# Kernel tuning notes

Measured on AMD Instinct MI355X. Metric: run time of the kernel, lower is better.

Reference implementation:

```python
import jax, jax.numpy as jnp
import numpy as np

W = 4           # cp_size (simulated ranks)
NUM_HEADS = 32
HEAD_SIZE = 128
NUM_KV_HEADS = 8
BLOCK_SIZE = 16
NUM_BLOCKS = 1024
MAX_BLOCKS = 32
MAX_CTX = 512   # <= _PARTITION_SIZE so single-partition stats are exact
NUM_SEQS = 32
SCALE = 1.0 / np.sqrt(HEAD_SIZE)
NEG_INF = -1e30


def setup_inputs() -> dict:
    key = jax.random.key(0)
    k1, k2, k3, k4, k5 = jax.random.split(key, 5)
    query = jax.random.normal(k1, (NUM_SEQS, 1, NUM_HEADS * HEAD_SIZE), dtype=jnp.float32)
    # per-rank paged KV caches, layout [W, num_blocks, kv_heads, block_size, head_size]
    key_cache = jax.random.normal(k2, (W, NUM_BLOCKS, NUM_KV_HEADS, BLOCK_SIZE, HEAD_SIZE), dtype=jnp.float32)
    value_cache = jax.random.normal(k3, (W, NUM_BLOCKS, NUM_KV_HEADS, BLOCK_SIZE, HEAD_SIZE), dtype=jnp.float32)
    block_tables = jax.random.randint(k4, (W, NUM_SEQS, MAX_BLOCKS), 0, NUM_BLOCKS, dtype=jnp.int32)
    context_lens = jax.random.randint(k5, (W, NUM_SEQS), 1, MAX_CTX + 1, dtype=jnp.int32)
    return {"query": query, "key_cache": key_cache, "value_cache": value_cache,
            "block_tables": block_tables, "context_lens": context_lens}


def reference(query, key_cache, value_cache, block_tables, context_lens):
    B, L, _ = query.shape
    S = B * L                       # num_seqs (decode: L=1)
    G = NUM_KV_HEADS
    Q = NUM_HEADS // G              # queries per kv head
    T = MAX_BLOCKS * BLOCK_SIZE     # max context per rank

    q = query.reshape(S, G, Q, HEAD_SIZE)
    ridx = jnp.arange(W)[:, None, None]
    # gather paged blocks: [W, S, MAX_BLOCKS, G, BLOCK_SIZE, D] -> [W, S, G, T, D]
    k = key_cache[ridx, block_tables].transpose(0, 1, 3, 2, 4, 5).reshape(W, S, G, T, HEAD_SIZE)
    v = value_cache[ridx, block_tables].transpose(0, 1, 3, 2, 4, 5).reshape(W, S, G, T, HEAD_SIZE)

    logits = jnp.einsum('sgqd,wsgtd->wsgqt', q, k) * SCALE
    mask = jnp.arange(T)[None, None, None, None, :] < context_lens[:, :, None, None, None]
    logits = jnp.where(mask, logits, NEG_INF)

    # per-rank online-softmax stats (== paged_attention_v2 single-partition output)
    m = jnp.max(logits, axis=-1)                      # [W,S,G,Q] max logit per rank
    p = jnp.exp(logits - m[..., None])
    p = jnp.where(mask, p, 0.0)
    esum = jnp.sum(p, axis=-1)                        # [W,S,G,Q]
    out_r = jnp.einsum('wsgqt,wsgtd->wsgqd', p, v) / esum[..., None]  # normalized per-rank out

    # cross-rank log-sum-exp reduction (distributed_paged_attention_v2_reduce)
    gmax = jnp.max(m, axis=0)                         # [S,G,Q]
    w_r = esum * jnp.exp(m - gmax[None])              # [W,S,G,Q]
    out = jnp.sum(out_r * w_r[..., None], axis=0) / jnp.sum(w_r, axis=0)[..., None]

    return out.reshape(B, L, NUM_HEADS * HEAD_SIZE)
```

## Files before the change

### kernel.cpp

```cpp
#include <hip/hip_runtime.h>
#include <math.h>

#define W 4
#define NUM_HEADS 32
#define HEAD_SIZE 128
#define G 8
#define QPG 4
#define BLOCK_SZ 16
#define NUM_BLOCKS 1024
#define MAX_BLOCKS 32
#define S 32
#define SCALE 0.08838834764831845f

template <bool FUSED>
__global__ __launch_bounds__(256)
void pa_partial_kernel(const float* __restrict__ query,
                       const float* __restrict__ key_cache,
                       const float* __restrict__ value_cache,
                       const int* __restrict__ block_tables,
                       const int* __restrict__ context_lens,
                       float* __restrict__ acc_ws,
                       float* __restrict__ m_ws,
                       float* __restrict__ e_ws,
                       float* __restrict__ out)
{
    const int bx = blockIdx.x;
    int s, g, w0, w1;
    if (FUSED) {
        s = bx / G; g = bx % G; w0 = 0; w1 = W;
    } else {
        g = bx % G;
        int t = bx / G;
        s = t % S;
        w0 = t / S; w1 = w0 + 1;
    }
    const int tid   = threadIdx.x;
    const int accid = tid >> 5;
    const int lane  = tid & 31;
    const int d0    = lane * 4;

    __shared__ int   bt_lds[MAX_BLOCKS];
    __shared__ float sm_m[8][QPG];
    __shared__ float sm_e[8][QPG];
    __shared__ float sm_acc[8][QPG][HEAD_SIZE];

    float4 qf[QPG];
#pragma unroll
    for (int qi = 0; qi < QPG; ++qi)
        qf[qi] = *reinterpret_cast<const float4*>(
            query + ((size_t)s * NUM_HEADS + g * QPG + qi) * HEAD_SIZE + d0);

    float  m_i[QPG], e_i[QPG];
    float4 acc[QPG];
#pragma unroll
    for (int qi = 0; qi < QPG; ++qi) {
        m_i[qi] = -INFINITY; e_i[qi] = 0.f;
        acc[qi] = make_float4(0.f, 0.f, 0.f, 0.f);
    }

    const size_t stride_blk = (size_t)G * BLOCK_SZ * HEAD_SIZE;

    for (int w = w0; w < w1; ++w) {
        __syncthreads();
        if (tid < MAX_BLOCKS)
            bt_lds[tid] = block_tables[((size_t)w * S + s) * MAX_BLOCKS + tid];
        __syncthreads();

        const int ctx = context_lens[w * S + s];
        const float* kbase = key_cache   + ((size_t)w * NUM_BLOCKS * G + g) * BLOCK_SZ * HEAD_SIZE;
        const float* vbase = value_cache + ((size_t)w * NUM_BLOCKS * G + g) * BLOCK_SZ * HEAD_SIZE;

        for (int t = accid; t < ctx; t += 8) {
            const int blk  = bt_lds[t >> 4];
            const int slot = t & (BLOCK_SZ - 1);
            const size_t off = (size_t)blk * stride_blk + (size_t)slot * HEAD_SIZE + d0;
            const float4 kx = *reinterpret_cast<const float4*>(kbase + off);
            const float4 vx = *reinterpret_cast<const float4*>(vbase + off);

            float4 dv;
            dv.x = qf[0].x * kx.x + qf[0].y * kx.y + qf[0].z * kx.z + qf[0].w * kx.w;
            dv.y = qf[1].x * kx.x + qf[1].y * kx.y + qf[1].z * kx.z + qf[1].w * kx.w;
            dv.z = qf[2].x * kx.x + qf[2].y * kx.y + qf[2].z * kx.z + qf[2].w * kx.w;
            dv.w = qf[3].x * kx.x + qf[3].y * kx.y + qf[3].z * kx.z + qf[3].w * kx.w;
#pragma unroll
            for (int o = 16; o > 0; o >>= 1) {
                dv.x += __shfl_xor(dv.x, o);
                dv.y += __shfl_xor(dv.y, o);
                dv.z += __shfl_xor(dv.z, o);
                dv.w += __shfl_xor(dv.w, o);
            }
            const float lg[QPG] = {dv.x * SCALE, dv.y * SCALE, dv.z * SCALE, dv.w * SCALE};
#pragma unroll
            for (int qi = 0; qi < QPG; ++qi) {
                const float mn    = fmaxf(m_i[qi], lg[qi]);
                const float alpha = __expf(m_i[qi] - mn);
                const float p     = __expf(lg[qi] - mn);
                m_i[qi] = mn;
                e_i[qi] = e_i[qi] * alpha + p;
                acc[qi].x = acc[qi].x * alpha + p * vx.x;
                acc[qi].y = acc[qi].y * alpha + p * vx.y;
                acc[qi].z = acc[qi].z * alpha + p * vx.z;
                acc[qi].w = acc[qi].w * alpha + p * vx.w;
            }
        }
    }

#pragma unroll
    for (int qi = 0; qi < QPG; ++qi) {
        if (lane == 0) { sm_m[accid][qi] = m_i[qi]; sm_e[accid][qi] = e_i[qi]; }
        sm_acc[accid][qi][d0 + 0] = acc[qi].x;
        sm_acc[accid][qi][d0 + 1] = acc[qi].y;
        sm_acc[accid][qi][d0 + 2] = acc[qi].z;
        sm_acc[accid][qi][d0 + 3] = acc[qi].w;
    }
    __syncthreads();

    for (int p = tid; p < QPG * HEAD_SIZE; p += 256) {
        const int qi = p >> 7;
        const int d  = p & (HEAD_SIZE - 1);
        float gm = -INFINITY;
#pragma unroll
        for (int h = 0; h < 8; ++h) gm = fmaxf(gm, sm_m[h][qi]);
        float num = 0.f, den = 0.f;
#pragma unroll
        for (int h = 0; h < 8; ++h) {
            const float sc = __expf(sm_m[h][qi] - gm);
            num += sm_acc[h][qi][d] * sc;
            den += sm_e[h][qi] * sc;
        }
        if (FUSED) {
            out[((size_t)s * NUM_HEADS + g * QPG + qi) * HEAD_SIZE + d] = num / den;
        } else {
            const size_t idx = (((size_t)w0 * S + s) * G + g) * QPG + qi;
            acc_ws[idx * HEAD_SIZE + d] = num;
            if (d == 0) { m_ws[idx] = gm; e_ws[idx] = den; }
        }
    }
}

__global__ __launch_bounds__(256)
void pa_reduce_kernel(const float* __restrict__ acc_ws,
                      const float* __restrict__ m_ws,
                      const float* __restrict__ e_ws,
                      float* __restrict__ out)
{
    const int bx = blockIdx.x;
    const int s = bx / G, g = bx % G;
    const int tid = threadIdx.x;
    for (int p = tid; p < QPG * HEAD_SIZE; p += 256) {
        const int qi = p >> 7;
        const int d  = p & (HEAD_SIZE - 1);
        float mw[W], ew[W];
        float gm = -INFINITY;
#pragma unroll
        for (int w = 0; w < W; ++w) {
            const size_t idx = (((size_t)w * S + s) * G + g) * QPG + qi;
            mw[w] = m_ws[idx];
            ew[w] = e_ws[idx];
            gm = fmaxf(gm, mw[w]);
        }
        float num = 0.f, den = 0.f;
#pragma unroll
        for (int w = 0; w < W; ++w) {
            const float sc = __expf(mw[w] - gm);
            const size_t idx = (((size_t)w * S + s) * G + g) * QPG + qi;
            num += acc_ws[idx * HEAD_SIZE + d] * sc;
            den += ew[w] * sc;
        }
        out[((size_t)s * NUM_HEADS + g * QPG + qi) * HEAD_SIZE + d] = num / den;
    }
}

extern "C" void kernel_launch(void* const* d_in, const int* in_sizes, int n_in,
                              void* d_out, int out_size, void* d_ws, size_t ws_size,
                              hipStream_t stream) {
    const float* query       = (const float*)d_in[0];
    const float* key_cache   = (const float*)d_in[1];
    const float* value_cache = (const float*)d_in[2];
    const int*   block_tables = (const int*)d_in[3];
    const int*   context_lens = (const int*)d_in[4];
    float* out = (float*)d_out;

    const size_t n_acc   = (size_t)W * S * G * QPG * HEAD_SIZE;
    const size_t n_stats = (size_t)W * S * G * QPG;
    const size_t need    = (n_acc + 2 * n_stats) * sizeof(float);

    if (ws_size >= need) {
        float* acc_ws = (float*)d_ws;
        float* m_ws   = acc_ws + n_acc;
        float* e_ws   = m_ws + n_stats;
        pa_partial_kernel<false><<<W * S * G, 256, 0, stream>>>(
            query, key_cache, value_cache, block_tables, context_lens,
            acc_ws, m_ws, e_ws, nullptr);
        pa_reduce_kernel<<<S * G, 256, 0, stream>>>(acc_ws, m_ws, e_ws, out);
    } else {
        pa_partial_kernel<true><<<S * G, 256, 0, stream>>>(
            query, key_cache, value_cache, block_tables, context_lens,
            nullptr, nullptr, nullptr, out);
    }
}
```

Baseline: 471.5 us.

## Split each rank's context across two workgroups and process two tokens per iteration

The partial kernel now launches SPLIT=2 workgroups per (rank, seq, kv-head), each taking an interleaved half of the tokens, and the reduce kernel combines 8 partitions instead of 4. Each warp handles two tokens per loop iteration with one combined online-softmax update, so more loads are in flight and fewer exp/rescale operations run per token. Launch bounds request 5 blocks per CU for occupancy. The cost is a larger workspace, more partial-output traffic and a wider reduction. The fused fallback becomes a separate kernel.

Result: no change. 463.7 us (-1.6%).

```diff
diff --git a/kernel.cpp b/kernel.cpp
--- a/kernel.cpp
+++ b/kernel.cpp
@@ -10,10 +10,15 @@
 #define NUM_BLOCKS 1024
 #define MAX_BLOCKS 32
 #define S 32
+#define SPLIT 2
+#define NPART (W * SPLIT)
 #define SCALE 0.08838834764831845f
-
-template <bool FUSED>
-__global__ __launch_bounds__(256)
+#define NEG_BIG (-1e30f)
+
+#define BLK_STRIDE (G * BLOCK_SZ * HEAD_SIZE)
+#define WG_STRIDE  (NUM_BLOCKS * BLK_STRIDE)
+
+__global__ __launch_bounds__(256, 5)
 void pa_partial_kernel(const float* __restrict__ query,
                        const float* __restrict__ key_cache,
                        const float* __restrict__ value_cache,
@@ -21,87 +26,94 @@
                        const int* __restrict__ context_lens,
                        float* __restrict__ acc_ws,
                        float* __restrict__ m_ws,
-                       float* __restrict__ e_ws,
-                       float* __restrict__ out)
+                       float* __restrict__ e_ws)
 {
-    const int bx = blockIdx.x;
-    int s, g, w0, w1;
-    if (FUSED) {
-        s = bx / G; g = bx % G; w0 = 0; w1 = W;
-    } else {
-        g = bx % G;
-        int t = bx / G;
-        s = t % S;
-        w0 = t / S; w1 = w0 + 1;
-    }
+    int bx = blockIdx.x;
+    const int p = bx % SPLIT; bx /= SPLIT;
+    const int g = bx % G;     bx /= G;
+    const int s = bx % S;
+    const int w = bx / S;
+
     const int tid   = threadIdx.x;
     const int accid = tid >> 5;
     const int lane  = tid & 31;
     const int d0    = lane * 4;
+    const int h     = accid + 8 * p;
 
     __shared__ int   bt_lds[MAX_BLOCKS];
     __shared__ float sm_m[8][QPG];
     __shared__ float sm_e[8][QPG];
     __shared__ float sm_acc[8][QPG][HEAD_SIZE];
 
+    if (tid < MAX_BLOCKS)
+        bt_lds[tid] = block_tables[((size_t)w * S + s) * MAX_BLOCKS + tid];
+    __syncthreads();
+
     float4 qf[QPG];
 #pragma unroll
     for (int qi = 0; qi < QPG; ++qi)
         qf[qi] = *reinterpret_cast<const float4*>(
             query + ((size_t)s * NUM_HEADS + g * QPG + qi) * HEAD_SIZE + d0);
 
+    const int ctx = context_lens[w * S + s];
+    const float* kbase = key_cache   + (size_t)w * WG_STRIDE + (size_t)g * BLOCK_SZ * HEAD_SIZE;
+    const float* vbase = value_cache + (size_t)w * WG_STRIDE + (size_t)g * BLOCK_SZ * HEAD_SIZE;
+
     float  m_i[QPG], e_i[QPG];
     float4 acc[QPG];
 #pragma unroll
     for (int qi = 0; qi < QPG; ++qi) {
-        m_i[qi] = -INFINITY; e_i[qi] = 0.f;
+        m_i[qi] = NEG_BIG; e_i[qi] = 0.f;
         acc[qi] = make_float4(0.f, 0.f, 0.f, 0.f);
     }
 
-    const size_t stride_blk = (size_t)G * BLOCK_SZ * HEAD_SIZE;
-
-    for (int w = w0; w < w1; ++w) {
-        __syncthreads();
-        if (tid < MAX_BLOCKS)
-            bt_lds[tid] = block_tables[((size_t)w * S + s) * MAX_BLOCKS + tid];
-        __syncthreads();
-
-        const int ctx = context_lens[w * S + s];
-        const float* kbase = key_cache   + ((size_t)w * NUM_BLOCKS * G + g) * BLOCK_SZ * HEAD_SIZE;
-        const float* vbase = value_cache + ((size_t)w * NUM_BLOCKS * G + g) * BLOCK_SZ * HEAD_SIZE;
-
-        for (int t = accid; t < ctx; t += 8) {
-            const int blk  = bt_lds[t >> 4];
-            const int slot = t & (BLOCK_SZ - 1);
-            const size_t off = (size_t)blk * stride_blk + (size_t)slot * HEAD_SIZE + d0;
-            const float4 kx = *reinterpret_cast<const float4*>(kbase + off);
-            const float4 vx = *reinterpret_cast<const float4*>(vbase + off);
-
-            float4 dv;
-            dv.x = qf[0].x * kx.x + qf[0].y * kx.y + qf[0].z * kx.z + qf[0].w * kx.w;
-            dv.y = qf[1].x * kx.x + qf[1].y * kx.y + qf[1].z * kx.z + qf[1].w * kx.w;
-            dv.z = qf[2].x * kx.x + qf[2].y * kx.y + qf[2].z * kx.z + qf[2].w * kx.w;
-            dv.w = qf[3].x * kx.x + qf[3].y * kx.y + qf[3].z * kx.z + qf[3].w * kx.w;
-#pragma unroll
-            for (int o = 16; o > 0; o >>= 1) {
-                dv.x += __shfl_xor(dv.x, o);
-                dv.y += __shfl_xor(dv.y, o);
-                dv.z += __shfl_xor(dv.z, o);
-                dv.w += __shfl_xor(dv.w, o);
-            }
-            const float lg[QPG] = {dv.x * SCALE, dv.y * SCALE, dv.z * SCALE, dv.w * SCALE};
-#pragma unroll
-            for (int qi = 0; qi < QPG; ++qi) {
-                const float mn    = fmaxf(m_i[qi], lg[qi]);
-                const float alpha = __expf(m_i[qi] - mn);
-                const float p     = __expf(lg[qi] - mn);
-                m_i[qi] = mn;
-                e_i[qi] = e_i[qi] * alpha + p;
-                acc[qi].x = acc[qi].x * alpha + p * vx.x;
-                acc[qi].y = acc[qi].y * alpha + p * vx.y;
-                acc[qi].z = acc[qi].z * alpha + p * vx.z;
-                acc[qi].w = acc[qi].w * alpha + p * vx.w;
-            }
+    for (int t = h; t < ctx; t += 2 * 16) {
+        const int off1 = bt_lds[t >> 4] * BLK_STRIDE + (t & 15) * HEAD_SIZE + d0;
+        const float4 k1 = *reinterpret_cast<const float4*>(kbase + off1);
+        const float4 v1 = *reinterpret_cast<const float4*>(vbase + off1);
+        const int  t2   = t + 16;
+        const bool vld2 = t2 < ctx;
+        float4 k2 = make_float4(0.f, 0.f, 0.f, 0.f);
+        float4 v2 = make_float4(0.f, 0.f, 0.f, 0.f);
+        if (vld2) {
+            const int off2 = bt_lds[t2 >> 4] * BLK_STRIDE + (t2 & 15) * HEAD_SIZE + d0;
+            k2 = *reinterpret_cast<const float4*>(kbase + off2);
+            v2 = *reinterpret_cast<const float4*>(vbase + off2);
+        }
+
+        float4 dv1, dv2;
+        dv1.x = qf[0].x*k1.x + qf[0].y*k1.y + qf[0].z*k1.z + qf[0].w*k1.w;
+        dv1.y = qf[1].x*k1.x + qf[1].y*k1.y + qf[1].z*k1.z + qf[1].w*k1.w;
+        dv1.z = qf[2].x*k1.x + qf[2].y*k1.y + qf[2].z*k1.z + qf[2].w*k1.w;
+        dv1.w = qf[3].x*k1.x + qf[3].y*k1.y + qf[3].z*k1.z + qf[3].w*k1.w;
+        dv2.x = qf[0].x*k2.x + qf[0].y*k2.y + qf[0].z*k2.z + qf[0].w*k2.w;
+        dv2.y = qf[1].x*k2.x + qf[1].y*k2.y + qf[1].z*k2.z + qf[1].w*k2.w;
+        dv2.z = qf[2].x*k2.x + qf[2].y*k2.y + qf[2].z*k2.z + qf[2].w*k2.w;
+        dv2.w = qf[3].x*k2.x + qf[3].y*k2.y + qf[3].z*k2.z + qf[3].w*k2.w;
+#pragma unroll
+        for (int o = 16; o > 0; o >>= 1) {
+            dv1.x += __shfl_xor(dv1.x, o); dv1.y += __shfl_xor(dv1.y, o);
+            dv1.z += __shfl_xor(dv1.z, o); dv1.w += __shfl_xor(dv1.w, o);
+            dv2.x += __shfl_xor(dv2.x, o); dv2.y += __shfl_xor(dv2.y, o);
+            dv2.z += __shfl_xor(dv2.z, o); dv2.w += __shfl_xor(dv2.w, o);
+        }
+        const float l1[QPG] = {dv1.x*SCALE, dv1.y*SCALE, dv1.z*SCALE, dv1.w*SCALE};
+        float l2[QPG] = {dv2.x*SCALE, dv2.y*SCALE, dv2.z*SCALE, dv2.w*SCALE};
+#pragma unroll
+        for (int qi = 0; qi < QPG; ++qi) if (!vld2) l2[qi] = NEG_BIG;
+
+#pragma unroll
+        for (int qi = 0; qi < QPG; ++qi) {
+            const float mn    = fmaxf(m_i[qi], fmaxf(l1[qi], l2[qi]));
+            const float alpha = __expf(m_i[qi] - mn);
+            const float p1    = __expf(l1[qi] - mn);
+            const float p2    = __expf(l2[qi] - mn);
+            m_i[qi] = mn;
+            e_i[qi] = e_i[qi] * alpha + (p1 + p2);
+            acc[qi].x = fmaf(acc[qi].x, alpha, fmaf(p1, v1.x, p2 * v2.x));
+            acc[qi].y = fmaf(acc[qi].y, alpha, fmaf(p1, v1.y, p2 * v2.y));
+            acc[qi].z = fmaf(acc[qi].z, alpha, fmaf(p1, v1.z, p2 * v2.z));
+            acc[qi].w = fmaf(acc[qi].w, alpha, fmaf(p1, v1.w, p2 * v2.w));
         }
     }
 
@@ -115,26 +127,23 @@
     }
     __syncthreads();
 
-    for (int p = tid; p < QPG * HEAD_SIZE; p += 256) {
-        const int qi = p >> 7;
-        const int d  = p & (HEAD_SIZE - 1);
-        float gm = -INFINITY;
-#pragma unroll
-        for (int h = 0; h < 8; ++h) gm = fmaxf(gm, sm_m[h][qi]);
+    const int r = w * SPLIT + p;
+    for (int pi = tid; pi < QPG * HEAD_SIZE; pi += 256) {
+        const int qi = pi >> 7;
+        const int d  = pi & (HEAD_SIZE - 1);
+        float gm = NEG_BIG;
+#pragma unroll
+        for (int hh = 0; hh < 8; ++hh) gm = fmaxf(gm, sm_m[hh][qi]);
         float num = 0.f, den = 0.f;
 #pragma unroll
-        for (int h = 0; h < 8; ++h) {
-            const float sc = __expf(sm_m[h][qi] - gm);
-            num += sm_acc[h][qi][d] * sc;
-            den += sm_e[h][qi] * sc;
-        }
-        if (FUSED) {
-            out[((size_t)s * NUM_HEADS + g * QPG + qi) * HEAD_SIZE + d] = num / den;
-        } else {
-            const size_t idx = (((size_t)w0 * S + s) * G + g) * QPG + qi;
-            acc_ws[idx * HEAD_SIZE + d] = num;
-            if (d == 0) { m_ws[idx] = gm; e_ws[idx] = den; }
-        }
+        for (int hh = 0; hh < 8; ++hh) {
+            const float sc = __expf(sm_m[hh][qi] - gm);
+            num += sm_acc[hh][qi][d] * sc;
+            den += sm_e[hh][qi] * sc;
+        }
+        const size_t idx = (((size_t)r * S + s) * G + g) * QPG + qi;
+        acc_ws[idx * HEAD_SIZE + d] = num;
+        if (d == 0) { m_ws[idx] = gm; e_ws[idx] = den; }
     }
 }
 
@@ -147,25 +156,124 @@
     const int bx = blockIdx.x;
     const int s = bx / G, g = bx % G;
     const int tid = threadIdx.x;
-    for (int p = tid; p < QPG * HEAD_SIZE; p += 256) {
-        const int qi = p >> 7;
-        const int d  = p & (HEAD_SIZE - 1);
-        float mw[W], ew[W];
-        float gm = -INFINITY;
-#pragma unroll
-        for (int w = 0; w < W; ++w) {
-            const size_t idx = (((size_t)w * S + s) * G + g) * QPG + qi;
-            mw[w] = m_ws[idx];
-            ew[w] = e_ws[idx];
-            gm = fmaxf(gm, mw[w]);
+    for (int pi = tid; pi < QPG * HEAD_SIZE; pi += 256) {
+        const int qi = pi >> 7;
+        const int d  = pi & (HEAD_SIZE - 1);
+        float mw[NPART], ew[NPART];
+        float gm = NEG_BIG;
+#pragma unroll
+        for (int r = 0; r < NPART; ++r) {
+            const size_t idx = (((size_t)r * S + s) * G + g) * QPG + qi;
+            mw[r] = m_ws[idx];
+            ew[r] = e_ws[idx];
+            gm = fmaxf(gm, mw[r]);
         }
         float num = 0.f, den = 0.f;
 #pragma unroll
-        for (int w = 0; w < W; ++w) {
-            const float sc = __expf(mw[w] - gm);
-            const size_t idx = (((size_t)w * S + s) * G + g) * QPG + qi;
+        for (int r = 0; r < NPART; ++r) {
+            const float sc = __expf(mw[r] - gm);
+            const size_t idx = (((size_t)r * S + s) * G + g) * QPG + qi;
             num += acc_ws[idx * HEAD_SIZE + d] * sc;
-            den += ew[w] * sc;
+            den += ew[r] * sc;
+        }
+        out[((size_t)s * NUM_HEADS + g * QPG + qi) * HEAD_SIZE + d] = num / den;
+    }
+}
+
+__global__ __launch_bounds__(256)
+void pa_fused_kernel(const float* __restrict__ query,
+                     const float* __restrict__ key_cache,
+                     const float* __restrict__ value_cache,
+                     const int* __restrict__ block_tables,
+                     const int* __restrict__ context_lens,
+                     float* __restrict__ out)
+{
+    const int bx = blockIdx.x;
+    const int s = bx / G, g = bx % G;
+    const int tid   = threadIdx.x;
+    const int accid = tid >> 5;
+    const int lane  = tid & 31;
+    const int d0    = lane * 4;
+
+    __shared__ int   bt_lds[MAX_BLOCKS];
+    __shared__ float sm_m[8][QPG];
+    __shared__ float sm_e[8][QPG];
+    __shared__ float sm_acc[8][QPG][HEAD_SIZE];
+
+    float4 qf[QPG];
+#pragma unroll
+    for (int qi = 0; qi < QPG; ++qi)
+        qf[qi] = *reinterpret_cast<const float4*>(
+            query + ((size_t)s * NUM_HEADS + g * QPG + qi) * HEAD_SIZE + d0);
+
+    float  m_i[QPG], e_i[QPG];
+    float4 acc[QPG];
+#pragma unroll
+    for (int qi = 0; qi < QPG; ++qi) {
+        m_i[qi] = NEG_BIG; e_i[qi] = 0.f;
+        acc[qi] = make_float4(0.f, 0.f, 0.f, 0.f);
+    }
+
+    for (int w = 0; w < W; ++w) {
+        __syncthreads();
+        if (tid < MAX_BLOCKS)
+            bt_lds[tid] = block_tables[((size_t)w * S + s) * MAX_BLOCKS + tid];
+        __syncthreads();
+        const int ctx = context_lens[w * S + s];
+        const float* kbase = key_cache   + (size_t)w * WG_STRIDE + (size_t)g * BLOCK_SZ * HEAD_SIZE;
+        const float* vbase = value_cache + (size_t)w * WG_STRIDE + (size_t)g * BLOCK_SZ * HEAD_SIZE;
+        for (int t = accid; t < ctx; t += 8) {
+            const int off = bt_lds[t >> 4] * BLK_STRIDE + (t & 15) * HEAD_SIZE + d0;
+            const float4 kx = *reinterpret_cast<const float4*>(kbase + off);
+            const float4 vx = *reinterpret_cast<const float4*>(vbase + off);
+            float4 dv;
+            dv.x = qf[0].x*kx.x + qf[0].y*kx.y + qf[0].z*kx.z + qf[0].w*kx.w;
+            dv.y = qf[1].x*kx.x + qf[1].y*kx.y + qf[1].z*kx.z + qf[1].w*kx.w;
+            dv.z = qf[2].x*kx.x + qf[2].y*kx.y + qf[2].z*kx.z + qf[2].w*kx.w;
+            dv.w = qf[3].x*kx.x + qf[3].y*kx.y + qf[3].z*kx.z + qf[3].w*kx.w;
+#pragma unroll
+            for (int o = 16; o > 0; o >>= 1) {
+                dv.x += __shfl_xor(dv.x, o); dv.y += __shfl_xor(dv.y, o);
+                dv.z += __shfl_xor(dv.z, o); dv.w += __shfl_xor(dv.w, o);
+            }
+            const float lg[QPG] = {dv.x*SCALE, dv.y*SCALE, dv.z*SCALE, dv.w*SCALE};
+#pragma unroll
+            for (int qi = 0; qi < QPG; ++qi) {
+                const float mn    = fmaxf(m_i[qi], lg[qi]);
+                const float alpha = __expf(m_i[qi] - mn);
+                const float pp    = __expf(lg[qi] - mn);
+                m_i[qi] = mn;
+                e_i[qi] = e_i[qi] * alpha + pp;
+                acc[qi].x = fmaf(acc[qi].x, alpha, pp * vx.x);
+                acc[qi].y = fmaf(acc[qi].y, alpha, pp * vx.y);
+                acc[qi].z = fmaf(acc[qi].z, alpha, pp * vx.z);
+                acc[qi].w = fmaf(acc[qi].w, alpha, pp * vx.w);
+            }
+        }
+    }
+
+#pragma unroll
+    for (int qi = 0; qi < QPG; ++qi) {
+        if (lane == 0) { sm_m[accid][qi] = m_i[qi]; sm_e[accid][qi] = e_i[qi]; }
+        sm_acc[accid][qi][d0 + 0] = acc[qi].x;
+        sm_acc[accid][qi][d0 + 1] = acc[qi].y;
+        sm_acc[accid][qi][d0 + 2] = acc[qi].z;
+        sm_acc[accid][qi][d0 + 3] = acc[qi].w;
+    }
+    __syncthreads();
+
+    for (int pi = tid; pi < QPG * HEAD_SIZE; pi += 256) {
+        const int qi = pi >> 7;
+        const int d  = pi & (HEAD_SIZE - 1);
+        float gm = NEG_BIG;
+#pragma unroll
+        for (int hh = 0; hh < 8; ++hh) gm = fmaxf(gm, sm_m[hh][qi]);
+        float num = 0.f, den = 0.f;
+#pragma unroll
+        for (int hh = 0; hh < 8; ++hh) {
+            const float sc = __expf(sm_m[hh][qi] - gm);
+            num += sm_acc[hh][qi][d] * sc;
+            den += sm_e[hh][qi] * sc;
         }
         out[((size_t)s * NUM_HEADS + g * QPG + qi) * HEAD_SIZE + d] = num / den;
     }
@@ -174,28 +282,27 @@
 extern "C" void kernel_launch(void* const* d_in, const int* in_sizes, int n_in,
                               void* d_out, int out_size, void* d_ws, size_t ws_size,
                               hipStream_t stream) {
-    const float* query       = (const float*)d_in[0];
-    const float* key_cache   = (const float*)d_in[1];
-    const float* value_cache = (const float*)d_in[2];
+    const float* query        = (const float*)d_in[0];
+    const float* key_cache    = (const float*)d_in[1];
+    const float* value_cache  = (const float*)d_in[2];
     const int*   block_tables = (const int*)d_in[3];
     const int*   context_lens = (const int*)d_in[4];
     float* out = (float*)d_out;
 
-    const size_t n_acc   = (size_t)W * S * G * QPG * HEAD_SIZE;
-    const size_t n_stats = (size_t)W * S * G * QPG;
+    const size_t n_acc   = (size_t)NPART * S * G * QPG * HEAD_SIZE;
+    const size_t n_stats = (size_t)NPART * S * G * QPG;
     const size_t need    = (n_acc + 2 * n_stats) * sizeof(float);
 
     if (ws_size >= need) {
         float* acc_ws = (float*)d_ws;
         float* m_ws   = acc_ws + n_acc;
         float* e_ws   = m_ws + n_stats;
-        pa_partial_kernel<false><<<W * S * G, 256, 0, stream>>>(
+        pa_partial_kernel<<<W * S * G * SPLIT, 256, 0, stream>>>(
             query, key_cache, value_cache, block_tables, context_lens,
-            acc_ws, m_ws, e_ws, nullptr);
+            acc_ws, m_ws, e_ws);
         pa_reduce_kernel<<<S * G, 256, 0, stream>>>(acc_ws, m_ws, e_ws, out);
     } else {
-        pa_partial_kernel<true><<<S * G, 256, 0, stream>>>(
-            query, key_cache, value_cache, block_tables, context_lens,
-            nullptr, nullptr, nullptr, out);
+        pa_fused_kernel<<<S * G, 256, 0, stream>>>(
+            query, key_cache, value_cache, block_tables, context_lens, out);
     }
 }
```
